# Optimization experiments

Hardware: AMD Instinct MI355X
Metric: run time of the kernel (lower is better)

The kernel has to match this reference:

```python
import jax, jax.numpy as jnp
import numpy as np

N_ENTITY = 30000
N_REL = 12
N_BASES = 8
KG_DIM = 128
TOK_DIM = 768
B = 32
N_CTX_ENT = 50
SEQ = 256
N_EDGES = 400000
VOCAB = 30522
PAD_IDX = 0


def setup_inputs() -> dict:
    key = jax.random.key(0)
    ks = jax.random.split(key, 24)
    s = 0.02
    inp = {
        "context_entities": jax.random.randint(ks[0], (B, N_CTX_ENT), 0, N_ENTITY),
        "context_tokens": jax.random.randint(ks[1], (B, SEQ), 0, VOCAB),
        "edge_index": jax.random.randint(ks[2], (2, N_EDGES), 0, N_ENTITY),
        "edge_type": jax.random.randint(ks[3], (N_EDGES,), 0, N_REL),
        # stand-in for bert_model(...).last_hidden_state
        "token_embedding": jax.random.normal(ks[4], (B, SEQ, TOK_DIM), dtype=jnp.float32),
        # RGCN basis-decomposition params (x=None -> node-identity features)
        "comp": jax.random.normal(ks[5], (N_REL, N_BASES), dtype=jnp.float32) * s,
        "basis": jax.random.normal(ks[6], (N_BASES, N_ENTITY, KG_DIM), dtype=jnp.float32) * s,
        "root": jax.random.normal(ks[7], (N_ENTITY, KG_DIM), dtype=jnp.float32) * s,
        "rgcn_bias": jnp.zeros((KG_DIM,), dtype=jnp.float32),
        # SelfDotAttention over entity reps (dim=da=KG_DIM)
        "ent_W": jax.random.normal(ks[8], (KG_DIM, KG_DIM), dtype=jnp.float32) * s,
        "ent_b": jnp.zeros((KG_DIM,), dtype=jnp.float32),
        "ent_v": jax.random.normal(ks[9], (KG_DIM,), dtype=jnp.float32) * s,
        # AdditiveAttention over token reps (dim=da=TOK_DIM)
        "tok_W": jax.random.normal(ks[10], (TOK_DIM, TOK_DIM), dtype=jnp.float32) * s,
        "tok_b": jnp.zeros((TOK_DIM,), dtype=jnp.float32),
        "tok_v": jax.random.normal(ks[11], (TOK_DIM,), dtype=jnp.float32) * s,
        # linear_transformation: token_emb_dim -> kg_emb_dim
        "lin_W": jax.random.normal(ks[12], (KG_DIM, TOK_DIM), dtype=jnp.float32) * s,
        "lin_b": jnp.zeros((KG_DIM,), dtype=jnp.float32),
        # gating: 2*kg_emb_dim -> kg_emb_dim
        "gate_W": jax.random.normal(ks[13], (KG_DIM, 2 * KG_DIM), dtype=jnp.float32) * s,
        "gate_b": jnp.zeros((KG_DIM,), dtype=jnp.float32),
    }
    return inp


def _rgcn(comp, basis, root, bias, edge_index, edge_type):
    # composed per-relation weight over identity features: [R, N, D]
    weight = jnp.einsum('rb,bnd->rnd', comp, basis)
    src, dst = edge_index[0], edge_index[1]
    msg = weight[edge_type, src]                      # [E, D] gather
    # per-relation, per-target mean aggregation (PyG RGCNConv aggr='mean')
    seg = edge_type * N_ENTITY + dst
    cnt = jax.ops.segment_sum(jnp.ones((msg.shape[0],), msg.dtype), seg,
                              num_segments=N_REL * N_ENTITY)
    norm = 1.0 / jnp.maximum(cnt[seg], 1.0)
    agg = jax.ops.segment_sum(msg * norm[:, None], dst, num_segments=N_ENTITY)
    return agg + root + bias                          # [N, D]


def _attn_pool(h, mask, W, b, v):
    # e = v^T tanh(h W + b); masked softmax; weighted sum over sequence
    e = jnp.einsum('bld,d->bl', jnp.tanh(jnp.einsum('bld,de->ble', h, W) + b), v)
    e = jnp.where(mask, e, jnp.asarray(-1e9, h.dtype))
    a = jax.nn.softmax(e, axis=-1)
    return jnp.einsum('bl,bld->bd', a, h)


def reference(context_entities, context_tokens, edge_index, edge_type,
              token_embedding, comp, basis, root, rgcn_bias,
              ent_W, ent_b, ent_v, tok_W, tok_b, tok_v,
              lin_W, lin_b, gate_W, gate_b):
    kg_embedding = _rgcn(comp, basis, root, rgcn_bias, edge_index, edge_type)

    entity_reps = kg_embedding[context_entities]              # [B, L_e, D]
    entity_mask = context_entities != PAD_IDX
    entity_attn_rep = _attn_pool(entity_reps, entity_mask, ent_W, ent_b, ent_v)

    token_mask = context_tokens != PAD_IDX
    token_attn_rep = _attn_pool(token_embedding, token_mask, tok_W, tok_b, tok_v)
    token_attn_rep = token_attn_rep @ lin_W.T + lin_b         # [B, D]

    gate = jax.nn.sigmoid(
        jnp.concatenate([token_attn_rep, entity_attn_rep], axis=1) @ gate_W.T + gate_b)
    user_embedding = gate * token_attn_rep + (1.0 - gate) * entity_attn_rep

    scores = user_embedding @ kg_embedding.T                  # [B, N_ENTITY]
    return scores
```

## Files before the change

kernel.cpp:

```cpp
#include <hip/hip_runtime.h>
#include <hip/hip_bf16.h>
#include <math.h>

#define N_ENTITY 30000
#define N_REL    12
#define N_BASES  8
#define KG_DIM   128
#define TOK_DIM  768
#define BATCH    32
#define N_CTX    50
#define SEQ      256
#define N_EDGES  400000

#define OFF_KG     0
#define OFF_CNT    3840000
#define OFF_DEG    4200000
#define OFF_START  4230000
#define OFF_CURSOR 4260004
#define OFF_CHUNK  4290004
#define OFF_SR     4290068
#define OFF_ETOK   5090068
#define OFF_ENT    5098260
#define OFF_TOK    5102356
#define OFF_USER   5106452
#define OFF_W      5110548
#define OFF_ABF    5110548
#define OFF_WBF    8256276
#define NEED_W_BYTES ((size_t)(OFF_W + 23040000) * 4)

typedef __bf16 bf16x8 __attribute__((ext_vector_type(8)));
typedef float  floatx4 __attribute__((ext_vector_type(4)));

__device__ __forceinline__ float tanh_fast(float x) {
    float ax = fabsf(x);
    float e = __expf(-2.0f * ax);
    float t = 1.0f - 2.0f * e / (1.0f + e);
    return copysignf(t, x);
}

__global__ void zero_kernel(int* __restrict__ p, int n) {
    int i = blockIdx.x * 256 + threadIdx.x;
    if (i < n) p[i] = 0;
}

__global__ void count_kernel(const int* __restrict__ edge_index,
                             const int* __restrict__ edge_type,
                             int* __restrict__ cnt) {
    int e = blockIdx.x * 256 + threadIdx.x;
    if (e >= N_EDGES) return;
    int r = edge_type[e];
    int dst = edge_index[N_EDGES + e];
    atomicAdd(&cnt[r * N_ENTITY + dst], 1);
}

__global__ __launch_bounds__(1024) void scan1_kernel(const int* __restrict__ cnt,
                                                     int* __restrict__ deg,
                                                     int* __restrict__ start,
                                                     int* __restrict__ chunksum) {
    __shared__ int wsum[16];
    int tid = threadIdx.x, lane = tid & 63, wv = tid >> 6;
    int i = blockIdx.x * 1024 + tid;
    int v = 0;
    if (i < N_ENTITY) {
#pragma unroll
        for (int r = 0; r < N_REL; ++r) v += cnt[r * N_ENTITY + i];
        deg[i] = v;
    }
    int x = v;
#pragma unroll
    for (int off = 1; off < 64; off <<= 1) {
        int t = __shfl_up(x, off);
        if (lane >= off) x += t;
    }
    if (lane == 63) wsum[wv] = x;
    __syncthreads();
    if (wv == 0 && lane < 16) {
        int w = wsum[lane];
#pragma unroll
        for (int off = 1; off < 16; off <<= 1) {
            int t = __shfl_up(w, off);
            if (lane >= off) w += t;
        }
        wsum[lane] = w;
    }
    __syncthreads();
    int wbase = (wv == 0) ? 0 : wsum[wv - 1];
    if (i < N_ENTITY) start[i] = wbase + x - v;
    if (tid == 1023) chunksum[blockIdx.x] = wbase + x;
}

__global__ void scan2_kernel(const int* __restrict__ chunksum,
                             int* __restrict__ chunkoff,
                             int* __restrict__ start) {
    int lane = threadIdx.x;
    int v = (lane < 30) ? chunksum[lane] : 0;
    int x = v;
#pragma unroll
    for (int off = 1; off < 64; off <<= 1) {
        int t = __shfl_up(x, off);
        if (lane >= off) x += t;
    }
    if (lane < 30) chunkoff[lane] = x - v;
    if (lane == 63) start[N_ENTITY] = x;
}

__global__ __launch_bounds__(1024) void scan3_kernel(const int* __restrict__ chunkoff,
                                                     int* __restrict__ start,
                                                     int* __restrict__ cursor) {
    int i = blockIdx.x * 1024 + threadIdx.x;
    if (i < N_ENTITY) {
        int s = start[i] + chunkoff[blockIdx.x];
        start[i] = s;
        cursor[i] = s;
    }
}

__global__ void place_kernel(const int* __restrict__ edge_index,
                             const int* __restrict__ edge_type,
                             const int* __restrict__ cnt,
                             int* __restrict__ cursor,
                             int2* __restrict__ er) {
    int e = blockIdx.x * 256 + threadIdx.x;
    if (e >= N_EDGES) return;
    int r = edge_type[e];
    int src = edge_index[e];
    int dst = edge_index[N_EDGES + e];
    int c = cnt[r * N_ENTITY + dst];
    float norm = 1.0f / (float)(c > 1 ? c : 1);
    int slot = atomicAdd(&cursor[dst], 1);
    er[slot] = make_int2(src | (r << 15), __float_as_int(norm));
}

__global__ void weight_bf16_kernel(const float* __restrict__ comp,
                                   const float4* __restrict__ basis4,
                                   uint2* __restrict__ w2) {
    int idx = blockIdx.x * 256 + threadIdx.x;
    float4 bv[N_BASES];
#pragma unroll
    for (int i = 0; i < N_BASES; ++i) bv[i] = basis4[(size_t)i * 960000 + idx];
#pragma unroll
    for (int r = 0; r < N_REL; ++r) {
        float s0 = 0.f, s1 = 0.f, s2 = 0.f, s3 = 0.f;
#pragma unroll
        for (int i = 0; i < N_BASES; ++i) {
            float c = comp[r * N_BASES + i];
            s0 += c * bv[i].x; s1 += c * bv[i].y;
            s2 += c * bv[i].z; s3 += c * bv[i].w;
        }
        union { __bf16 h[4]; uint2 u; } pk;
        pk.h[0] = (__bf16)s0; pk.h[1] = (__bf16)s1;
        pk.h[2] = (__bf16)s2; pk.h[3] = (__bf16)s3;
        w2[(size_t)r * 960000 + idx] = pk.u;
    }
}

__global__ __launch_bounds__(256) void gather_kernel(const int* __restrict__ start,
                                                     const int* __restrict__ deg,
                                                     const int2* __restrict__ er,
                                                     const unsigned int* __restrict__ w,
                                                     const float2* __restrict__ root2,
                                                     const float2* __restrict__ bias2,
                                                     float2* __restrict__ kg2) {
    int wv = threadIdx.x >> 6, lane = threadIdx.x & 63;
    int dst = blockIdx.x * 4 + wv;
    if (dst >= N_ENTITY) return;
    int s = start[dst], n = deg[dst];
    float ax = 0.f, ay = 0.f;
    int j = 0;
    for (; j + 1 < n; j += 2) {
        int2 e0 = er[s + j], e1 = er[s + j + 1];
        float n0 = __int_as_float(e0.y), n1 = __int_as_float(e1.y);
        int s0 = e0.x & 32767, r0 = e0.x >> 15;
        int s1 = e1.x & 32767, r1 = e1.x >> 15;
        unsigned int u0 = w[((size_t)(r0 * N_ENTITY + s0) << 6) + lane];
        unsigned int u1 = w[((size_t)(r1 * N_ENTITY + s1) << 6) + lane];
        ax += __uint_as_float(u0 << 16) * n0 + __uint_as_float(u1 << 16) * n1;
        ay += __uint_as_float(u0 & 0xffff0000u) * n0 +
              __uint_as_float(u1 & 0xffff0000u) * n1;
    }
    if (j < n) {
        int2 e0 = er[s + j];
        float n0 = __int_as_float(e0.y);
        int s0 = e0.x & 32767, r0 = e0.x >> 15;
        unsigned int u0 = w[((size_t)(r0 * N_ENTITY + s0) << 6) + lane];
        ax += __uint_as_float(u0 << 16) * n0;
        ay += __uint_as_float(u0 & 0xffff0000u) * n0;
    }
    float2 rt = root2[(size_t)dst * 64 + lane];
    float2 bs = bias2[lane];
    kg2[(size_t)dst * 64 + lane] = make_float2(ax + rt.x + bs.x, ay + rt.y + bs.y);
}

__global__ __launch_bounds__(256) void gather_otf_kernel(const int* __restrict__ start,
                                                         const int* __restrict__ deg,
                                                         const int2* __restrict__ er,
                                                         const float* __restrict__ comp,
                                                         const float2* __restrict__ basis2,
                                                         const float2* __restrict__ root2,
                                                         const float2* __restrict__ bias2,
                                                         float2* __restrict__ kg2) {
    int wv = threadIdx.x >> 6, lane = threadIdx.x & 63;
    int dst = blockIdx.x * 4 + wv;
    if (dst >= N_ENTITY) return;
    int s = start[dst], n = deg[dst];
    float ax = 0.f, ay = 0.f;
    for (int j = 0; j < n; ++j) {
        int2 e0 = er[s + j];
        float nm = __int_as_float(e0.y);
        int src = e0.x & 32767, r = e0.x >> 15;
        float mx = 0.f, my = 0.f;
#pragma unroll
        for (int b = 0; b < N_BASES; ++b) {
            float cf = comp[r * N_BASES + b];
            float2 bs = basis2[((size_t)b * N_ENTITY + src) * 64 + lane];
            mx += cf * bs.x; my += cf * bs.y;
        }
        ax += mx * nm; ay += my * nm;
    }
    float2 rt = root2[(size_t)dst * 64 + lane];
    float2 bs = bias2[lane];
    kg2[(size_t)dst * 64 + lane] = make_float2(ax + rt.x + bs.x, ay + rt.y + bs.y);
}

__global__ __launch_bounds__(256) void ent_attn_kernel(const int* __restrict__ ctx_ent,
                                                       const float* __restrict__ kg,
                                                       const float* __restrict__ W,
                                                       const float* __restrict__ bb,
                                                       const float* __restrict__ v,
                                                       float* __restrict__ ent_rep) {
    __shared__ __align__(16) float Ws[KG_DIM * KG_DIM];
    __shared__ __align__(16) float h[N_CTX * KG_DIM];
    __shared__ float es[64];
    __shared__ int ids[N_CTX];
    int b = blockIdx.x, tid = threadIdx.x;
    if (tid < N_CTX) ids[tid] = ctx_ent[b * N_CTX + tid];
    __syncthreads();
    for (int i = tid; i < N_CTX * 32; i += 256) {
        int l = i >> 5, d4 = i & 31;
        ((float4*)h)[i] = ((const float4*)kg)[(size_t)ids[l] * 32 + d4];
    }
    for (int i = tid; i < KG_DIM * KG_DIM / 4; i += 256)
        ((float4*)Ws)[i] = ((const float4*)W)[i];
    __syncthreads();

    int wave = tid >> 6, lane = tid & 63;
    const int nl = (N_CTX - wave + 3) / 4;
    float s0[13], s1[13];
#pragma unroll
    for (int i = 0; i < 13; ++i) { s0[i] = 0.f; s1[i] = 0.f; }
    for (int k4 = 0; k4 < 32; ++k4) {
        float4 hk[13];
#pragma unroll
        for (int i = 0; i < 13; ++i)
            if (i < nl) hk[i] = ((const float4*)h)[(wave + i * 4) * 32 + k4];
#pragma unroll
        for (int kk = 0; kk < 4; ++kk) {
            int k = k4 * 4 + kk;
            float w0 = Ws[k * KG_DIM + lane];
            float w1 = Ws[k * KG_DIM + lane + 64];
#pragma unroll
            for (int i = 0; i < 13; ++i) {
                if (i < nl) {
                    float hv = (&hk[i].x)[kk];
                    s0[i] += hv * w0;
                    s1[i] += hv * w1;
                }
            }
        }
    }
    float bias0 = bb[lane], bias1 = bb[lane + 64];
    float v0 = v[lane], v1 = v[lane + 64];
    for (int i = 0; i < nl; ++i) {
        int l = wave + i * 4;
        float p = tanhf(s0[i] + bias0) * v0 + tanhf(s1[i] + bias1) * v1;
        p += __shfl_xor(p, 32); p += __shfl_xor(p, 16); p += __shfl_xor(p, 8);
        p += __shfl_xor(p, 4);  p += __shfl_xor(p, 2);  p += __shfl_xor(p, 1);
        if (lane == 0) es[l] = p;
    }
    __syncthreads();
    if (tid < 64) {
        float val = (tid < N_CTX && ids[tid] != 0) ? es[tid] : -1e9f;
        float mx = val;
        mx = fmaxf(mx, __shfl_xor(mx, 32)); mx = fmaxf(mx, __shfl_xor(mx, 16));
        mx = fmaxf(mx, __shfl_xor(mx, 8));  mx = fmaxf(mx, __shfl_xor(mx, 4));
        mx = fmaxf(mx, __shfl_xor(mx, 2));  mx = fmaxf(mx, __shfl_xor(mx, 1));
        float ex = (tid < N_CTX) ? expf(val - mx) : 0.f;
        float sm = ex;
        sm += __shfl_xor(sm, 32); sm += __shfl_xor(sm, 16); sm += __shfl_xor(sm, 8);
        sm += __shfl_xor(sm, 4);  sm += __shfl_xor(sm, 2);  sm += __shfl_xor(sm, 1);
        if (tid < N_CTX) es[tid] = ex / sm;
    }
    __syncthreads();
    if (tid < KG_DIM) {
        float o = 0.f;
#pragma unroll
        for (int l = 0; l < N_CTX; ++l) o += es[l] * h[l * KG_DIM + tid];
        ent_rep[b * KG_DIM + tid] = o;
    }
}


__global__ void convA_kernel(const float* __restrict__ in, __bf16* __restrict__ out,
                             int n8) {
    int i = blockIdx.x * 256 + threadIdx.x;
    if (i >= n8) return;
    const float4* p = (const float4*)(in + (size_t)i * 8);
    float4 a = p[0], b = p[1];
    union { __bf16 h[8]; uint4 u; } r;
    r.h[0] = (__bf16)a.x; r.h[1] = (__bf16)a.y; r.h[2] = (__bf16)a.z; r.h[3] = (__bf16)a.w;
    r.h[4] = (__bf16)b.x; r.h[5] = (__bf16)b.y; r.h[6] = (__bf16)b.z; r.h[7] = (__bf16)b.w;
    *(uint4*)(out + (size_t)i * 8) = r.u;
}

__global__ void convWT_kernel(const float* __restrict__ W, __bf16* __restrict__ Wt) {
    __shared__ float tile[64][65];
    int tx = threadIdx.x & 63, ty = threadIdx.x >> 6;
    int kb = blockIdx.x * 64, cb = blockIdx.y * 64;
#pragma unroll
    for (int i = 0; i < 16; ++i) {
        int r = ty + i * 4;
        tile[r][tx] = W[(size_t)(kb + r) * TOK_DIM + cb + tx];
    }
    __syncthreads();
#pragma unroll
    for (int i = 0; i < 16; ++i) {
        int r = ty + i * 4;
        Wt[(size_t)(cb + r) * TOK_DIM + kb + tx] = (__bf16)tile[tx][r];
    }
}

__global__ __launch_bounds__(256) void tok_gemm_kernel(const __bf16* __restrict__ A,
                                                       const __bf16* __restrict__ Bt,
                                                       const float* __restrict__ bias,
                                                       const float* __restrict__ v,
                                                       float* __restrict__ e_out) {
    __shared__ __align__(16) __bf16 sA[4096];
    __shared__ __align__(16) __bf16 sB[4096];
    int tid = threadIdx.x;
    int wave = tid >> 6, lane = tid & 63;
    int wm = wave >> 1, wn = wave & 1;
    int quad = lane >> 4, idx = lane & 15;
    int m0 = blockIdx.y * 128, c0 = blockIdx.x * 128;

    int rowS = tid & 127, kpS = tid >> 7;
    const __bf16* gA0 = A + (size_t)(m0 + rowS) * TOK_DIM + kpS * 8;
    const __bf16* gA1 = gA0 + 16;
    const __bf16* gB0 = Bt + (size_t)(c0 + rowS) * TOK_DIM + kpS * 8;
    const __bf16* gB1 = gB0 + 16;
    __bf16* dA0 = &sA[tid * 8];
    __bf16* dA1 = &sA[tid * 8 + 2048];
    __bf16* dB0 = &sB[tid * 8];
    __bf16* dB1 = &sB[tid * 8 + 2048];

    floatx4 acc[4][4];
#pragma unroll
    for (int mi = 0; mi < 4; ++mi)
#pragma unroll
        for (int ni = 0; ni < 4; ++ni)
            acc[mi][ni] = (floatx4){0.f, 0.f, 0.f, 0.f};

    for (int k0 = 0; k0 < TOK_DIM; k0 += 32) {
        uint4 ra0 = *(const uint4*)(gA0 + k0);
        uint4 ra1 = *(const uint4*)(gA1 + k0);
        uint4 rb0 = *(const uint4*)(gB0 + k0);
        uint4 rb1 = *(const uint4*)(gB1 + k0);
        __syncthreads();
        *(uint4*)dA0 = ra0; *(uint4*)dA1 = ra1;
        *(uint4*)dB0 = rb0; *(uint4*)dB1 = rb1;
        __syncthreads();
        bf16x8 aF[4], bF[4];
#pragma unroll
        for (int i = 0; i < 4; ++i) {
            aF[i] = *(const bf16x8*)&sA[quad * 1024 + (wm * 64 + i * 16 + idx) * 8];
            bF[i] = *(const bf16x8*)&sB[quad * 1024 + (wn * 64 + i * 16 + idx) * 8];
        }
#pragma unroll
        for (int mi = 0; mi < 4; ++mi)
#pragma unroll
            for (int ni = 0; ni < 4; ++ni)
                acc[mi][ni] = __builtin_amdgcn_mfma_f32_16x16x32_bf16(
                    aF[mi], bF[ni], acc[mi][ni], 0, 0, 0);
    }

    float bv[4], vv[4];
#pragma unroll
    for (int ni = 0; ni < 4; ++ni) {
        int c = c0 + wn * 64 + ni * 16 + idx;
        bv[ni] = bias[c]; vv[ni] = v[c];
    }
#pragma unroll
    for (int mi = 0; mi < 4; ++mi) {
        float s[4] = {0.f, 0.f, 0.f, 0.f};
#pragma unroll
        for (int ni = 0; ni < 4; ++ni)
#pragma unroll
            for (int r = 0; r < 4; ++r)
                s[r] += tanh_fast(acc[mi][ni][r] + bv[ni]) * vv[ni];
#pragma unroll
        for (int r = 0; r < 4; ++r) {
            s[r] += __shfl_xor(s[r], 1); s[r] += __shfl_xor(s[r], 2);
            s[r] += __shfl_xor(s[r], 4); s[r] += __shfl_xor(s[r], 8);
        }
        if (idx == 0) {
            int rbase = m0 + wm * 64 + mi * 16 + quad * 4;
#pragma unroll
            for (int r = 0; r < 4; ++r) atomicAdd(&e_out[rbase + r], s[r]);
        }
    }
}

__global__ __launch_bounds__(256) void tok_pool2_kernel(const int* __restrict__ ctx_tok,
                                                        const float* __restrict__ e_ws,
                                                        const float4* __restrict__ emb4,
                                                        const float* __restrict__ lin_W,
                                                        float* __restrict__ tok_rep) {
    __shared__ float a_s[SEQ];
    __shared__ float4 part[8][32];
    __shared__ __align__(16) float pooled[128];
    __shared__ float redm[4];
    __shared__ float reds[4];
    int b = blockIdx.x, c = blockIdx.y;
    int tid = threadIdx.x;
    int wave = tid >> 6, lane = tid & 63;
    int t = ctx_tok[b * SEQ + tid];
    float val = (t != 0) ? e_ws[b * SEQ + tid] : -1e9f;
    float mx = val;
    mx = fmaxf(mx, __shfl_xor(mx, 32)); mx = fmaxf(mx, __shfl_xor(mx, 16));
    mx = fmaxf(mx, __shfl_xor(mx, 8));  mx = fmaxf(mx, __shfl_xor(mx, 4));
    mx = fmaxf(mx, __shfl_xor(mx, 2));  mx = fmaxf(mx, __shfl_xor(mx, 1));
    if (lane == 0) redm[wave] = mx;
    __syncthreads();
    mx = fmaxf(fmaxf(redm[0], redm[1]), fmaxf(redm[2], redm[3]));
    float ex = expf(val - mx);
    float sm = ex;
    sm += __shfl_xor(sm, 32); sm += __shfl_xor(sm, 16); sm += __shfl_xor(sm, 8);
    sm += __shfl_xor(sm, 4);  sm += __shfl_xor(sm, 2);  sm += __shfl_xor(sm, 1);
    if (lane == 0) reds[wave] = sm;
    __syncthreads();
    sm = reds[0] + reds[1] + reds[2] + reds[3];
    a_s[tid] = ex / sm;
    __syncthreads();
    int d4 = tid & 31, lg = tid >> 5;
    const float4* eb = emb4 + (size_t)b * SEQ * 192 + c * 32 + d4;
    float4 acc = make_float4(0.f, 0.f, 0.f, 0.f);
    for (int l = lg; l < SEQ; l += 8) {
        float al = a_s[l];
        float4 e = eb[(size_t)l * 192];
        acc.x += al * e.x; acc.y += al * e.y; acc.z += al * e.z; acc.w += al * e.w;
    }
    part[lg][d4] = acc;
    __syncthreads();
    if (tid < 32) {
        float4 s = part[0][tid];
#pragma unroll
        for (int g = 1; g < 8; ++g) {
            float4 p = part[g][tid];
            s.x += p.x; s.y += p.y; s.z += p.z; s.w += p.w;
        }
        ((float4*)pooled)[tid] = s;
    }
    __syncthreads();
    int d = tid & 127, hf = tid >> 7;
    const float* wr = lin_W + (size_t)d * TOK_DIM + c * 128 + hf * 64;
    float s = 0.f;
#pragma unroll 8
    for (int k = 0; k < 64; ++k) s += pooled[hf * 64 + k] * wr[k];
    atomicAdd(&tok_rep[b * KG_DIM + d], s);
}

__global__ void gate_kernel(const float* __restrict__ tok_rep,
                            const float* __restrict__ lin_b,
                            const float* __restrict__ ent_rep,
                            const float* __restrict__ gate_W,
                            const float* __restrict__ gate_b,
                            float* __restrict__ user) {
    __shared__ float tr[KG_DIM], er[KG_DIM];
    int b = blockIdx.x, d = threadIdx.x;
    tr[d] = tok_rep[b * KG_DIM + d] + lin_b[d];
    er[d] = ent_rep[b * KG_DIM + d];
    __syncthreads();
    float g = gate_b[d];
    const float* wr = gate_W + (size_t)d * 256;
#pragma unroll 8
    for (int k = 0; k < KG_DIM; ++k) g += tr[k] * wr[k] + er[k] * wr[KG_DIM + k];
    float sig = 1.f / (1.f + expf(-g));
    user[b * KG_DIM + d] = sig * tr[d] + (1.f - sig) * er[d];
}

__global__ void scores_kernel(const float* __restrict__ user,
                              const float4* __restrict__ kg4,
                              float* __restrict__ out) {
    __shared__ float4 u4[BATCH * 32];
    int tid = threadIdx.x;
    for (int i = tid; i < BATCH * 32; i += 256) u4[i] = ((const float4*)user)[i];
    __syncthreads();
    int n = blockIdx.x * 256 + tid;
    if (n >= N_ENTITY) return;
    float acc[BATCH];
#pragma unroll
    for (int b = 0; b < BATCH; ++b) acc[b] = 0.f;
    for (int d4 = 0; d4 < 32; ++d4) {
        float4 k = kg4[(size_t)n * 32 + d4];
#pragma unroll
        for (int b = 0; b < BATCH; ++b) {
            float4 u = u4[b * 32 + d4];
            acc[b] += k.x * u.x + k.y * u.y + k.z * u.z + k.w * u.w;
        }
    }
    for (int b = 0; b < BATCH; ++b) out[(size_t)b * N_ENTITY + n] = acc[b];
}

extern "C" void kernel_launch(void* const* d_in, const int* in_sizes, int n_in,
                              void* d_out, int out_size, void* d_ws, size_t ws_size,
                              hipStream_t stream) {
    (void)in_sizes; (void)n_in; (void)out_size;
    const int*   ctx_ent   = (const int*)d_in[0];
    const int*   ctx_tok   = (const int*)d_in[1];
    const int*   edge_index= (const int*)d_in[2];
    const int*   edge_type = (const int*)d_in[3];
    const float* tok_emb   = (const float*)d_in[4];
    const float* comp      = (const float*)d_in[5];
    const float* basis     = (const float*)d_in[6];
    const float* root      = (const float*)d_in[7];
    const float* rgcn_bias = (const float*)d_in[8];
    const float* ent_W     = (const float*)d_in[9];
    const float* ent_b     = (const float*)d_in[10];
    const float* ent_v     = (const float*)d_in[11];
    const float* tok_W     = (const float*)d_in[12];
    const float* tok_b     = (const float*)d_in[13];
    const float* tok_v     = (const float*)d_in[14];
    const float* lin_W     = (const float*)d_in[15];
    const float* lin_b     = (const float*)d_in[16];
    const float* gate_W    = (const float*)d_in[17];
    const float* gate_b    = (const float*)d_in[18];
    float* scores = (float*)d_out;

    float* ws = (float*)d_ws;
    float* kg      = ws + OFF_KG;
    int*   cnt     = (int*)(ws + OFF_CNT);
    int*   deg     = (int*)(ws + OFF_DEG);
    int*   start   = (int*)(ws + OFF_START);
    int*   cursor  = (int*)(ws + OFF_CURSOR);
    int*   chunk   = (int*)(ws + OFF_CHUNK);
    int2*  er      = (int2*)(ws + OFF_SR);
    float* e_ws    = ws + OFF_ETOK;
    float* ent_rep = ws + OFF_ENT;
    float* tok_rep = ws + OFF_TOK;
    float* user    = ws + OFF_USER;
    float* weight  = ws + OFF_W;
    __bf16* Abf    = (__bf16*)(ws + OFF_ABF);
    __bf16* Wbf    = (__bf16*)(ws + OFF_WBF);
    const bool use_weight = (ws_size >= NEED_W_BYTES);

    zero_kernel<<<(360000 + 255) / 256, 256, 0, stream>>>(cnt, 360000);
    count_kernel<<<(N_EDGES + 255) / 256, 256, 0, stream>>>(edge_index, edge_type, cnt);
    scan1_kernel<<<30, 1024, 0, stream>>>(cnt, deg, start, chunk);
    scan2_kernel<<<1, 64, 0, stream>>>(chunk, chunk + 32, start);
    scan3_kernel<<<30, 1024, 0, stream>>>(chunk + 32, start, cursor);
    place_kernel<<<(N_EDGES + 255) / 256, 256, 0, stream>>>(edge_index, edge_type, cnt,
                                                            cursor, er);
    zero_kernel<<<80, 256, 0, stream>>>((int*)e_ws, 20480);
    if (use_weight) {
        weight_bf16_kernel<<<3750, 256, 0, stream>>>(comp, (const float4*)basis,
                                                     (uint2*)weight);
        gather_kernel<<<(N_ENTITY + 3) / 4, 256, 0, stream>>>(
            start, deg, er, (const unsigned int*)weight, (const float2*)root,
            (const float2*)rgcn_bias, (float2*)kg);
    } else {
        gather_otf_kernel<<<(N_ENTITY + 3) / 4, 256, 0, stream>>>(
            start, deg, er, comp, (const float2*)basis, (const float2*)root,
            (const float2*)rgcn_bias, (float2*)kg);
    }
    ent_attn_kernel<<<BATCH, 256, 0, stream>>>(ctx_ent, kg, ent_W, ent_b, ent_v, ent_rep);

    convA_kernel<<<(BATCH * SEQ * TOK_DIM / 8 + 255) / 256, 256, 0, stream>>>(
        tok_emb, Abf, BATCH * SEQ * TOK_DIM / 8);
    {
        dim3 g(12, 12);
        convWT_kernel<<<g, 256, 0, stream>>>(tok_W, Wbf);
    }
    {
        dim3 g(TOK_DIM / 128, BATCH * SEQ / 128);
        tok_gemm_kernel<<<g, 256, 0, stream>>>(Abf, Wbf, tok_b, tok_v, e_ws);
    }
    {
        dim3 g(BATCH, 6);
        tok_pool2_kernel<<<g, 256, 0, stream>>>(ctx_tok, e_ws, (const float4*)tok_emb,
                                                lin_W, tok_rep);
    }
    gate_kernel<<<BATCH, 128, 0, stream>>>(tok_rep, lin_b, ent_rep, gate_W, gate_b, user);
    scores_kernel<<<(N_ENTITY + 255) / 256, 256, 0, stream>>>(user, (const float4*)kg, scores);
}
```

Before: 480.3 us.

## Store composed RGCN weights in scaled FP8, pool from bf16 tokens, fuse zeroing

The composed per-relation weight table is now packed to scaled FP8 instead of bf16, halving the bytes written by the weight kernel and read by the edge gather. The token pooling kernel reads the bf16 copy of the token embeddings instead of the fp32 original. The separate zeroing launch is folded into the scan2 kernel. These cut memory traffic and one launch, at the cost of a real precision loss in the RGCN aggregation (FP8 with a fixed 1024 scale) and bf16 rounding in pooling.

```diff
diff --git a/kernel.cpp b/kernel.cpp
--- a/kernel.cpp
+++ b/kernel.cpp
@@ -11,6 +11,9 @@
 #define N_CTX    50
 #define SEQ      256
 #define N_EDGES  400000
+
+#define W8_SCALE 1024.0f
+#define W8_INV   (1.0f / 1024.0f)
 
 #define OFF_KG     0
 #define OFF_CNT    3840000
@@ -26,7 +29,7 @@
 #define OFF_W      5110548
 #define OFF_ABF    5110548
 #define OFF_WBF    8256276
-#define NEED_W_BYTES ((size_t)(OFF_W + 23040000) * 4)
+#define NEED_W_BYTES ((size_t)(OFF_W + 11520000) * 4)
 
 typedef __bf16 bf16x8 __attribute__((ext_vector_type(8)));
 typedef float  floatx4 __attribute__((ext_vector_type(4)));
@@ -89,19 +92,24 @@
     if (tid == 1023) chunksum[blockIdx.x] = wbase + x;
 }
 
-__global__ void scan2_kernel(const int* __restrict__ chunksum,
-                             int* __restrict__ chunkoff,
-                             int* __restrict__ start) {
-    int lane = threadIdx.x;
-    int v = (lane < 30) ? chunksum[lane] : 0;
-    int x = v;
-#pragma unroll
-    for (int off = 1; off < 64; off <<= 1) {
-        int t = __shfl_up(x, off);
-        if (lane >= off) x += t;
-    }
-    if (lane < 30) chunkoff[lane] = x - v;
-    if (lane == 63) start[N_ENTITY] = x;
+__global__ __launch_bounds__(256) void scan2_kernel(const int* __restrict__ chunksum,
+                                                    int* __restrict__ chunkoff,
+                                                    int* __restrict__ start,
+                                                    int* __restrict__ zp) {
+    int tid = threadIdx.x;
+    if (tid < 64) {
+        int lane = tid;
+        int v = (lane < 30) ? chunksum[lane] : 0;
+        int x = v;
+#pragma unroll
+        for (int off = 1; off < 64; off <<= 1) {
+            int t = __shfl_up(x, off);
+            if (lane >= off) x += t;
+        }
+        if (lane < 30) chunkoff[lane] = x - v;
+        if (lane == 63) start[N_ENTITY] = x;
+    }
+    for (int i = tid; i < 20480; i += 256) zp[i] = 0;
 }
 
 __global__ __launch_bounds__(1024) void scan3_kernel(const int* __restrict__ chunkoff,
@@ -131,9 +139,9 @@
     er[slot] = make_int2(src | (r << 15), __float_as_int(norm));
 }
 
-__global__ void weight_bf16_kernel(const float* __restrict__ comp,
-                                   const float4* __restrict__ basis4,
-                                   uint2* __restrict__ w2) {
+__global__ void weight_fp8_kernel(const float* __restrict__ comp,
+                                  const float4* __restrict__ basis4,
+                                  unsigned int* __restrict__ w1) {
     int idx = blockIdx.x * 256 + threadIdx.x;
     float4 bv[N_BASES];
 #pragma unroll
@@ -147,17 +155,16 @@
             s0 += c * bv[i].x; s1 += c * bv[i].y;
             s2 += c * bv[i].z; s3 += c * bv[i].w;
         }
-        union { __bf16 h[4]; uint2 u; } pk;
-        pk.h[0] = (__bf16)s0; pk.h[1] = (__bf16)s1;
-        pk.h[2] = (__bf16)s2; pk.h[3] = (__bf16)s3;
-        w2[(size_t)r * 960000 + idx] = pk.u;
+        int pk = __builtin_amdgcn_cvt_pk_fp8_f32(s0 * W8_SCALE, s1 * W8_SCALE, 0, false);
+        pk = __builtin_amdgcn_cvt_pk_fp8_f32(s2 * W8_SCALE, s3 * W8_SCALE, pk, true);
+        w1[(size_t)r * 960000 + idx] = (unsigned int)pk;
     }
 }
 
 __global__ __launch_bounds__(256) void gather_kernel(const int* __restrict__ start,
                                                      const int* __restrict__ deg,
                                                      const int2* __restrict__ er,
-                                                     const unsigned int* __restrict__ w,
+                                                     const unsigned short* __restrict__ w8,
                                                      const float2* __restrict__ root2,
                                                      const float2* __restrict__ bias2,
                                                      float2* __restrict__ kg2) {
@@ -172,23 +179,25 @@
         float n0 = __int_as_float(e0.y), n1 = __int_as_float(e1.y);
         int s0 = e0.x & 32767, r0 = e0.x >> 15;
         int s1 = e1.x & 32767, r1 = e1.x >> 15;
-        unsigned int u0 = w[((size_t)(r0 * N_ENTITY + s0) << 6) + lane];
-        unsigned int u1 = w[((size_t)(r1 * N_ENTITY + s1) << 6) + lane];
-        ax += __uint_as_float(u0 << 16) * n0 + __uint_as_float(u1 << 16) * n1;
-        ay += __uint_as_float(u0 & 0xffff0000u) * n0 +
-              __uint_as_float(u1 & 0xffff0000u) * n1;
+        int u0 = (int)w8[((size_t)(r0 * N_ENTITY + s0) << 6) + lane];
+        int u1 = (int)w8[((size_t)(r1 * N_ENTITY + s1) << 6) + lane];
+        ax += __builtin_amdgcn_cvt_f32_fp8(u0, 0) * n0 +
+              __builtin_amdgcn_cvt_f32_fp8(u1, 0) * n1;
+        ay += __builtin_amdgcn_cvt_f32_fp8(u0, 1) * n0 +
+              __builtin_amdgcn_cvt_f32_fp8(u1, 1) * n1;
     }
     if (j < n) {
         int2 e0 = er[s + j];
         float n0 = __int_as_float(e0.y);
         int s0 = e0.x & 32767, r0 = e0.x >> 15;
-        unsigned int u0 = w[((size_t)(r0 * N_ENTITY + s0) << 6) + lane];
-        ax += __uint_as_float(u0 << 16) * n0;
-        ay += __uint_as_float(u0 & 0xffff0000u) * n0;
+        int u0 = (int)w8[((size_t)(r0 * N_ENTITY + s0) << 6) + lane];
+        ax += __builtin_amdgcn_cvt_f32_fp8(u0, 0) * n0;
+        ay += __builtin_amdgcn_cvt_f32_fp8(u0, 1) * n0;
     }
     float2 rt = root2[(size_t)dst * 64 + lane];
     float2 bs = bias2[lane];
-    kg2[(size_t)dst * 64 + lane] = make_float2(ax + rt.x + bs.x, ay + rt.y + bs.y);
+    kg2[(size_t)dst * 64 + lane] = make_float2(ax * W8_INV + rt.x + bs.x,
+                                               ay * W8_INV + rt.y + bs.y);
 }
 
 __global__ __launch_bounds__(256) void gather_otf_kernel(const int* __restrict__ start,
@@ -411,7 +420,7 @@
 
 __global__ __launch_bounds__(256) void tok_pool2_kernel(const int* __restrict__ ctx_tok,
                                                         const float* __restrict__ e_ws,
-                                                        const float4* __restrict__ emb4,
+                                                        const __bf16* __restrict__ Abf,
                                                         const float* __restrict__ lin_W,
                                                         float* __restrict__ tok_rep) {
     __shared__ float a_s[SEQ];
@@ -441,12 +450,17 @@
     a_s[tid] = ex / sm;
     __syncthreads();
     int d4 = tid & 31, lg = tid >> 5;
-    const float4* eb = emb4 + (size_t)b * SEQ * 192 + c * 32 + d4;
+    const unsigned int* eb = (const unsigned int*)(Abf + (size_t)b * SEQ * TOK_DIM +
+                                                   c * 128 + d4 * 4);
     float4 acc = make_float4(0.f, 0.f, 0.f, 0.f);
     for (int l = lg; l < SEQ; l += 8) {
         float al = a_s[l];
-        float4 e = eb[(size_t)l * 192];
-        acc.x += al * e.x; acc.y += al * e.y; acc.z += al * e.z; acc.w += al * e.w;
+        unsigned int u0 = eb[(size_t)l * 384];
+        unsigned int u1 = eb[(size_t)l * 384 + 1];
+        acc.x += al * __uint_as_float(u0 << 16);
+        acc.y += al * __uint_as_float(u0 & 0xffff0000u);
+        acc.z += al * __uint_as_float(u1 << 16);
+        acc.w += al * __uint_as_float(u1 & 0xffff0000u);
     }
     part[lg][d4] = acc;
     __syncthreads();
@@ -555,16 +569,15 @@
     zero_kernel<<<(360000 + 255) / 256, 256, 0, stream>>>(cnt, 360000);
     count_kernel<<<(N_EDGES + 255) / 256, 256, 0, stream>>>(edge_index, edge_type, cnt);
     scan1_kernel<<<30, 1024, 0, stream>>>(cnt, deg, start, chunk);
-    scan2_kernel<<<1, 64, 0, stream>>>(chunk, chunk + 32, start);
+    scan2_kernel<<<1, 256, 0, stream>>>(chunk, chunk + 32, start, (int*)e_ws);
     scan3_kernel<<<30, 1024, 0, stream>>>(chunk + 32, start, cursor);
     place_kernel<<<(N_EDGES + 255) / 256, 256, 0, stream>>>(edge_index, edge_type, cnt,
                                                             cursor, er);
-    zero_kernel<<<80, 256, 0, stream>>>((int*)e_ws, 20480);
     if (use_weight) {
-        weight_bf16_kernel<<<3750, 256, 0, stream>>>(comp, (const float4*)basis,
-                                                     (uint2*)weight);
+        weight_fp8_kernel<<<3750, 256, 0, stream>>>(comp, (const float4*)basis,
+                                                    (unsigned int*)weight);
         gather_kernel<<<(N_ENTITY + 3) / 4, 256, 0, stream>>>(
-            start, deg, er, (const unsigned int*)weight, (const float2*)root,
+            start, deg, er, (const unsigned short*)weight, (const float2*)root,
             (const float2*)rgcn_bias, (float2*)kg);
     } else {
         gather_otf_kernel<<<(N_ENTITY + 3) / 4, 256, 0, stream>>>(
@@ -585,8 +598,7 @@
     }
     {
         dim3 g(BATCH, 6);
-        tok_pool2_kernel<<<g, 256, 0, stream>>>(ctx_tok, e_ws, (const float4*)tok_emb,
-                                                lin_W, tok_rep);
+        tok_pool2_kernel<<<g, 256, 0, stream>>>(ctx_tok, e_ws, Abf, lin_W, tok_rep);
     }
     gate_kernel<<<BATCH, 128, 0, stream>>>(tok_rep, lin_b, ent_rep, gate_W, gate_b, user);
     scores_kernel<<<(N_ENTITY + 255) / 256, 256, 0, stream>>>(user, (const float4*)kg, scores);
```

New measurement: 473.2 us. Within noise of the previous version (-1.5%).
